# Optimization experiments

Hardware: AMD Instinct MI355X
Metric: run time of the kernel (lower is better)

Reference implementation:

```python
import jax, jax.numpy as jnp
import numpy as np

B, T, D_MODEL, H = 2, 2048, 1024, 16
D_HEAD = D_MODEL // H


def setup_inputs() -> dict:
    key = jax.random.key(0)
    k1, k2, k3 = jax.random.split(key, 3)
    x = jax.random.normal(k1, (B, T, D_MODEL), dtype=jnp.float32)
    # Linear weights stored as (in, out); scale like torch default init roughly
    W_qkv = jax.random.normal(k2, (D_MODEL, 3 * D_MODEL), dtype=jnp.float32) / np.sqrt(D_MODEL)
    W_o = jax.random.normal(k3, (D_MODEL, D_MODEL), dtype=jnp.float32) / np.sqrt(D_MODEL)
    return {"x": x, "W_qkv": W_qkv, "W_o": W_o}


def reference(x, W_qkv, W_o):
    Bx, Tx, C = x.shape
    qkv = x @ W_qkv                                   # (B,T,3C)
    qkv = qkv.reshape(Bx, Tx, 3, H, D_HEAD)
    q = qkv[:, :, 0].transpose(0, 2, 1, 3)            # (B,H,T,D)
    k = qkv[:, :, 1].transpose(0, 2, 1, 3)
    v = qkv[:, :, 2].transpose(0, 2, 1, 3)
    scale = 1.0 / np.sqrt(D_HEAD).astype(np.float32)
    att = jnp.einsum('bhqd,bhkd->bhqk', q, k) * scale  # (B,H,T,T)
    causal = jnp.tril(jnp.ones((Tx, Tx), dtype=bool))
    att = jnp.where(causal[None, None], att, jnp.float32(-jnp.inf))
    w = jax.nn.softmax(att, axis=-1)
    out = jnp.einsum('bhqk,bhkd->bhqd', w, v)          # (B,H,T,D)
    out = out.transpose(0, 2, 1, 3).reshape(Bx, Tx, C)
    return out @ W_o
```

## Files before the change

kernel.cpp:

```cpp
#include <hip/hip_runtime.h>

typedef unsigned short u16;
typedef unsigned int u32;
typedef __bf16 bf16x8 __attribute__((ext_vector_type(8)));
typedef float f32x4 __attribute__((ext_vector_type(4)));

#define DEV __device__ __forceinline__

constexpr int BB = 2;
constexpr int TT = 2048;
constexpr int CD = 1024;
constexpr int HH = 16;
constexpr int DH = 64;
constexpr int BT = BB * TT;

#define QSCALE 0.18033688011112042f

DEV u16 f2bf(float f) {
    u32 u = __builtin_bit_cast(u32, f);
    u32 r = u + 0x7FFFu + ((u >> 16) & 1u);
    return (u16)(r >> 16);
}

DEV f32x4 mfma16(bf16x8 a, bf16x8 b, f32x4 c) {
    return __builtin_amdgcn_mfma_f32_16x16x32_bf16(a, b, c, 0, 0, 0);
}

DEV void gld_lds16(u16* lds, const u16* g) {
    __builtin_amdgcn_global_load_lds(
        (const __attribute__((address_space(1))) unsigned int*)g,
        (__attribute__((address_space(3))) unsigned int*)lds, 16, 0, 0);
}

__global__ __launch_bounds__(256)
void prep_kernel(const float* __restrict__ x, u16* __restrict__ xb,
                 const float* __restrict__ Wqkv, u16* __restrict__ WqkvT,
                 const float* __restrict__ Wo, u16* __restrict__ WoT) {
    const int tid = threadIdx.x;
    int blk = blockIdx.x;
    if (blk < 2048) {
        const int i = (blk * 256 + tid) * 8;
        float4 a = *(const float4*)&x[i];
        float4 b = *(const float4*)&x[i + 4];
        u16 t[8];
        t[0] = f2bf(a.x); t[1] = f2bf(a.y); t[2] = f2bf(a.z); t[3] = f2bf(a.w);
        t[4] = f2bf(b.x); t[5] = f2bf(b.y); t[6] = f2bf(b.z); t[7] = f2bf(b.w);
        *(uint4*)&xb[i] = *(const uint4*)t;
        return;
    }
    __shared__ u16 tile[32][33];
    const float* in; u16* out; int rows, cols, bx, by;
    if (blk < 5120) { blk -= 2048; in = Wqkv; out = WqkvT; rows = 1024; cols = 3072; bx = blk % 96; by = blk / 96; }
    else            { blk -= 5120; in = Wo;   out = WoT;   rows = 1024; cols = 1024; bx = blk % 32; by = blk / 32; }
    const int c0 = bx * 32, r0 = by * 32;
    const int tx = tid & 31, ty = tid >> 5;
    #pragma unroll
    for (int i = ty; i < 32; i += 8)
        tile[i][tx] = f2bf(in[(r0 + i) * cols + (c0 + tx)]);
    __syncthreads();
    #pragma unroll
    for (int i = ty; i < 32; i += 8)
        out[(c0 + i) * rows + (r0 + tx)] = tile[tx][i];
}

template <int EPI, int BN, int GX>
__global__ __launch_bounds__(256)
void gemm_db(const u16* __restrict__ A, const u16* __restrict__ Bt,
             u16* __restrict__ out0, u16* __restrict__ out1,
             u16* __restrict__ out2, float* __restrict__ outf,
             int M, int N, int K) {
    constexpr int BM = 128, BK = 32, AST = 32;
    constexpr int NT = BN / 32;
    constexpr int NBLK = GX * 32;
    constexpr int CPX = NBLK / 8;
    __shared__ alignas(16) u16 As[2][BM * AST];
    __shared__ alignas(16) u16 Bs[2][BN * AST];

    const int tid  = threadIdx.x;
    const int wave = tid >> 6, lane = tid & 63;
    const int quad = lane >> 4, l16 = lane & 15;
    const int wm = (wave & 1) * 64, wn = (wave >> 1) * (BN / 2);

    int bid = (int)blockIdx.x;
    bid = (bid & 7) * CPX + (bid >> 3);
    const int bx = bid % GX, by = bid / GX;
    const int m0 = by * BM, n0 = bx * BN;

    const int srowA = wave * 32 + (lane >> 2);
    const int srowB = wave * (BN / 4) + (lane >> 2);
    const int scol  = (lane & 3) * 8;
    const u16* ga0 = A  + (size_t)(m0 + srowA) * K + scol;
    const u16* ga1 = ga0 + (size_t)16 * K;
    const u16* gb0 = Bt + (size_t)(n0 + srowB) * K + scol;
    const u16* gb1 = gb0 + (size_t)16 * K;

    auto stage = [&](int buf, int k0) {
        gld_lds16(&As[buf][wave * 1024],           ga0 + k0);
        gld_lds16(&As[buf][wave * 1024 + 512],     ga1 + k0);
        gld_lds16(&Bs[buf][wave * (BN * 8)],       gb0 + k0);
        if constexpr (BN == 128)
            gld_lds16(&Bs[buf][wave * (BN * 8) + 512], gb1 + k0);
    };

    f32x4 acc[4][NT] = {};

    stage(0, 0);
    __syncthreads();

    int cur = 0;
    for (int k0 = 0; k0 < K; k0 += BK, cur ^= 1) {
        if (k0 + BK < K) stage(cur ^ 1, k0 + BK);

        bf16x8 fa[4], fb[NT];
        #pragma unroll
        for (int mt = 0; mt < 4; ++mt)
            fa[mt] = *(const bf16x8*)&As[cur][(wm + mt * 16 + l16) * AST + quad * 8];
        #pragma unroll
        for (int nt = 0; nt < NT; ++nt)
            fb[nt] = *(const bf16x8*)&Bs[cur][(wn + nt * 16 + l16) * AST + quad * 8];
        #pragma unroll
        for (int mt = 0; mt < 4; ++mt)
            #pragma unroll
            for (int nt = 0; nt < NT; ++nt)
                acc[mt][nt] = mfma16(fa[mt], fb[nt], acc[mt][nt]);
        __syncthreads();
    }

    #pragma unroll
    for (int mt = 0; mt < 4; ++mt) {
        #pragma unroll
        for (int nt = 0; nt < NT; ++nt) {
            #pragma unroll
            for (int reg = 0; reg < 4; ++reg) {
                const int r = m0 + wm + mt * 16 + quad * 4 + reg;
                const int c = n0 + wn + nt * 16 + l16;
                if (EPI == 0) {
                    outf[(size_t)r * N + c] = acc[mt][nt][reg];
                } else {
                    const int which = c >> 10;
                    const int cc = c & 1023;
                    const int h = cc >> 6, d = cc & 63;
                    const int b = r >> 11, t = r & 2047;
                    const int bh = b * HH + h;
                    if (which == 0) {
                        out0[((size_t)bh * TT + t) * DH + d] =
                            f2bf(acc[mt][nt][reg] * QSCALE);
                    } else if (which == 1) {
                        out1[((size_t)bh * TT + t) * DH + d] = f2bf(acc[mt][nt][reg]);
                    } else {
                        out2[((size_t)bh * DH + d) * TT + t] = f2bf(acc[mt][nt][reg]);
                    }
                }
            }
        }
    }
}

constexpr int KST = 72;

DEV void attn_step(const bf16x8 fk[4][2], const bf16x8 fv[2][4],
                   const bf16x8* fq, f32x4* Oacc,
                   float& m_i, float& l_i, bool diag,
                   int wave, int quad, int l16) {
    f32x4 st[4];
    #pragma unroll
    for (int nt = 0; nt < 4; ++nt) {
        f32x4 t = {};
        t = mfma16(fk[nt][0], fq[0], t);
        t = mfma16(fk[nt][1], fq[1], t);
        st[nt] = t;
    }

    if (diag) {
        const int qg = wave * 16 + l16;
        #pragma unroll
        for (int nt = 0; nt < 4; ++nt)
            #pragma unroll
            for (int reg = 0; reg < 4; ++reg) {
                const int kg = nt * 16 + quad * 4 + reg;
                st[nt][reg] = (kg <= qg) ? st[nt][reg] : -INFINITY;
            }
    }

    float vmax = st[0][0];
    #pragma unroll
    for (int nt = 0; nt < 4; ++nt)
        #pragma unroll
        for (int reg = 0; reg < 4; ++reg)
            vmax = fmaxf(vmax, st[nt][reg]);
    vmax = fmaxf(vmax, __shfl_xor(vmax, 16, 64));
    vmax = fmaxf(vmax, __shfl_xor(vmax, 32, 64));

    const float mnew = fmaxf(m_i, vmax);
    const float alpha = __builtin_amdgcn_exp2f(m_i - mnew);
    m_i = mnew;

    float vsum = 0.f;
    #pragma unroll
    for (int nt = 0; nt < 4; ++nt)
        #pragma unroll
        for (int reg = 0; reg < 4; ++reg) {
            const float p = __builtin_amdgcn_exp2f(st[nt][reg] - mnew);
            st[nt][reg] = p;
            vsum += p;
        }
    vsum += __shfl_xor(vsum, 16, 64);
    vsum += __shfl_xor(vsum, 32, 64);
    l_i = l_i * alpha + vsum;

    #pragma unroll
    for (int dt = 0; dt < 4; ++dt)
        #pragma unroll
        for (int reg = 0; reg < 4; ++reg)
            Oacc[dt][reg] *= alpha;

    #pragma unroll
    for (int pair = 0; pair < 2; ++pair) {
        u16 pa[8];
        #pragma unroll
        for (int j = 0; j < 4; ++j) {
            pa[j]     = f2bf(st[2 * pair][j]);
            pa[4 + j] = f2bf(st[2 * pair + 1][j]);
        }
        const bf16x8 pb = *(const bf16x8*)pa;
        #pragma unroll
        for (int dt = 0; dt < 4; ++dt)
            Oacc[dt] = mfma16(fv[pair][dt], pb, Oacc[dt]);
    }
}

__global__ __launch_bounds__(256, 2)
void attn_kernel(const u16* __restrict__ Q, const u16* __restrict__ Kb,
                 const u16* __restrict__ Vt, u16* __restrict__ O) {
    __shared__ alignas(16) u16 Ks[2][64 * KST];
    __shared__ alignas(16) u16 Vs[2][64 * KST];

    const int p = blockIdx.x;
    const int bh = blockIdx.y;
    const int qtA = 31 - p;
    const int qtB = p;
    const int jmax = qtA;

    const int tid = threadIdx.x;
    const int wave = tid >> 6, lane = tid & 63;
    const int quad = lane >> 4, l16 = lane & 15;

    const u16* Qh = Q  + (size_t)bh * TT * DH;
    const u16* Kh = Kb + (size_t)bh * TT * DH;
    const u16* Vh = Vt + (size_t)bh * DH * TT;

    const int rowA = qtA * 64 + wave * 16;
    const int rowB = qtB * 64 + wave * 16;

    bf16x8 fqA[2], fqB[2];
    fqA[0] = *(const bf16x8*)&Qh[(rowA + l16) * DH + quad * 8];
    fqA[1] = *(const bf16x8*)&Qh[(rowA + l16) * DH + 32 + quad * 8];
    fqB[0] = *(const bf16x8*)&Qh[(rowB + l16) * DH + quad * 8];
    fqB[1] = *(const bf16x8*)&Qh[(rowB + l16) * DH + 32 + quad * 8];

    f32x4 OA[4] = {}, OB[4] = {};
    float mA = -INFINITY, lA = 0.f, mB = -INFINITY, lB = 0.f;

    const int trow = tid >> 3;
    const int ic   = tid & 7;
    const int tcol = ic * 8;
    const int vc1 = 32 * (ic >> 2) + 16 * (ic & 1) + 4 * ((ic & 3) >> 1);
    uint4 kr0, kr1, vr0, vr1;

    auto load_chunk = [&](int j) {
        const u16* ks = Kh + (size_t)j * 64 * DH;
        kr0 = *(const uint4*)&ks[trow * DH + tcol];
        kr1 = *(const uint4*)&ks[(trow + 32) * DH + tcol];
        const u16* vs = Vh + (size_t)j * 64;
        vr0 = *(const uint4*)&vs[(size_t)trow * TT + tcol];
        vr1 = *(const uint4*)&vs[(size_t)(trow + 32) * TT + tcol];
    };
    auto write_chunk = [&](int buf) {
        *(uint4*)&Ks[buf][trow * KST + tcol]        = kr0;
        *(uint4*)&Ks[buf][(trow + 32) * KST + tcol] = kr1;
        *(uint2*)&Vs[buf][trow * KST + vc1]            = *(const uint2*)&vr0;
        *(uint2*)&Vs[buf][trow * KST + vc1 + 8]        = *((const uint2*)&vr0 + 1);
        *(uint2*)&Vs[buf][(trow + 32) * KST + vc1]     = *(const uint2*)&vr1;
        *(uint2*)&Vs[buf][(trow + 32) * KST + vc1 + 8] = *((const uint2*)&vr1 + 1);
    };

    load_chunk(0);
    write_chunk(0);

    for (int j = 0; j <= jmax; ++j) {
        const int cur = j & 1;
        __syncthreads();
        if (j < jmax) load_chunk(j + 1);

        bf16x8 fk[4][2], fv[2][4];
        #pragma unroll
        for (int nt = 0; nt < 4; ++nt) {
            fk[nt][0] = *(const bf16x8*)&Ks[cur][(nt * 16 + l16) * KST + quad * 8];
            fk[nt][1] = *(const bf16x8*)&Ks[cur][(nt * 16 + l16) * KST + 32 + quad * 8];
        }
        #pragma unroll
        for (int pair = 0; pair < 2; ++pair)
            #pragma unroll
            for (int dt = 0; dt < 4; ++dt)
                fv[pair][dt] = *(const bf16x8*)
                    &Vs[cur][(dt * 16 + l16) * KST + pair * 32 + quad * 8];

        attn_step(fk, fv, fqA, OA, mA, lA, (j == qtA), wave, quad, l16);
        if (j <= qtB)
            attn_step(fk, fv, fqB, OB, mB, lB, (j == qtB), wave, quad, l16);
        if (j < jmax) write_chunk(cur ^ 1);
    }

    const int b = bh >> 4, h = bh & 15;
    const float rA = 1.f / lA, rB = 1.f / lB;
    #pragma unroll
    for (int dt = 0; dt < 4; ++dt) {
        u16 oa[4], ob[4];
        #pragma unroll
        for (int reg = 0; reg < 4; ++reg) {
            oa[reg] = f2bf(OA[dt][reg] * rA);
            ob[reg] = f2bf(OB[dt][reg] * rB);
        }
        *(uint2*)&O[((size_t)(b * TT + rowA + l16)) * CD + h * DH + dt * 16 + quad * 4] =
            *(const uint2*)oa;
        *(uint2*)&O[((size_t)(b * TT + rowB + l16)) * CD + h * DH + dt * 16 + quad * 4] =
            *(const uint2*)ob;
    }
}

extern "C" void kernel_launch(void* const* d_in, const int* in_sizes, int n_in,
                              void* d_out, int out_size, void* d_ws, size_t ws_size,
                              hipStream_t stream) {
    (void)in_sizes; (void)n_in; (void)out_size; (void)ws_size;
    const float* x    = (const float*)d_in[0];
    const float* Wqkv = (const float*)d_in[1];
    const float* Wo   = (const float*)d_in[2];
    float* out = (float*)d_out;

    char* ws = (char*)d_ws;
    u16* xb    = (u16*)(ws + 0);
    u16* WqkvT = (u16*)(ws + (8u  << 20));
    u16* WoT   = (u16*)(ws + (14u << 20));
    u16* Qb    = (u16*)(ws + (16u << 20));
    u16* Kb    = (u16*)(ws + (24u << 20));
    u16* Vt    = (u16*)(ws + (32u << 20));
    u16* attn  = (u16*)(ws + (40u << 20));

    prep_kernel<<<6144, 256, 0, stream>>>(x, xb, Wqkv, WqkvT, Wo, WoT);

    gemm_db<1, 128, 24><<<768, 256, 0, stream>>>(
        xb, WqkvT, Qb, Kb, Vt, nullptr, BT, 3072, CD);

    attn_kernel<<<dim3(16, BB * HH), 256, 0, stream>>>(Qb, Kb, Vt, attn);

    gemm_db<0, 64, 16><<<512, 256, 0, stream>>>(
        attn, WoT, nullptr, nullptr, nullptr, out, BT, CD, CD);
}
```

Before: 185.9 us.

## Split paired-tile attention blocks into single-tile blocks ordered longest-first

The attention kernel stops pairing two query tiles (qt and 31-qt) per block. It launches 1024 single-tile blocks, ordered so the longest causal tiles go first, and interleaves heads across block indices. Launch bounds go from 2 to 4 blocks per CU to raise occupancy. The softmax max and sum reductions become tree reductions to shorten dependency chains, and the float-to-bf16 conversion uses the native cast. This trades the K/V chunk reuse that came from sharing loads across two tiles for more parallelism and load balance through scheduling order, and it risks register pressure under the tighter launch bound.

```diff
diff --git a/kernel.cpp b/kernel.cpp
--- a/kernel.cpp
+++ b/kernel.cpp
@@ -17,9 +17,7 @@
 #define QSCALE 0.18033688011112042f
 
 DEV u16 f2bf(float f) {
-    u32 u = __builtin_bit_cast(u32, f);
-    u32 r = u + 0x7FFFu + ((u >> 16) & 1u);
-    return (u16)(r >> 16);
+    return __builtin_bit_cast(u16, (__bf16)f);
 }
 
 DEV f32x4 mfma16(bf16x8 a, bf16x8 b, f32x4 c) {
@@ -182,12 +180,18 @@
             }
     }
 
-    float vmax = st[0][0];
+    float v[16];
     #pragma unroll
     for (int nt = 0; nt < 4; ++nt)
         #pragma unroll
         for (int reg = 0; reg < 4; ++reg)
-            vmax = fmaxf(vmax, st[nt][reg]);
+            v[nt * 4 + reg] = st[nt][reg];
+    #pragma unroll
+    for (int s = 8; s > 0; s >>= 1)
+        #pragma unroll
+        for (int i = 0; i < s; ++i)
+            v[i] = fmaxf(v[i], v[i + s]);
+    float vmax = v[0];
     vmax = fmaxf(vmax, __shfl_xor(vmax, 16, 64));
     vmax = fmaxf(vmax, __shfl_xor(vmax, 32, 64));
 
@@ -195,15 +199,20 @@
     const float alpha = __builtin_amdgcn_exp2f(m_i - mnew);
     m_i = mnew;
 
-    float vsum = 0.f;
     #pragma unroll
     for (int nt = 0; nt < 4; ++nt)
         #pragma unroll
         for (int reg = 0; reg < 4; ++reg) {
             const float p = __builtin_amdgcn_exp2f(st[nt][reg] - mnew);
             st[nt][reg] = p;
-            vsum += p;
+            v[nt * 4 + reg] = p;
         }
+    #pragma unroll
+    for (int s = 8; s > 0; s >>= 1)
+        #pragma unroll
+        for (int i = 0; i < s; ++i)
+            v[i] += v[i + s];
+    float vsum = v[0];
     vsum += __shfl_xor(vsum, 16, 64);
     vsum += __shfl_xor(vsum, 32, 64);
     l_i = l_i * alpha + vsum;
@@ -216,30 +225,29 @@
 
     #pragma unroll
     for (int pair = 0; pair < 2; ++pair) {
-        u16 pa[8];
+        bf16x8 pb;
         #pragma unroll
         for (int j = 0; j < 4; ++j) {
-            pa[j]     = f2bf(st[2 * pair][j]);
-            pa[4 + j] = f2bf(st[2 * pair + 1][j]);
+            pb[j]     = (__bf16)st[2 * pair][j];
+            pb[4 + j] = (__bf16)st[2 * pair + 1][j];
         }
-        const bf16x8 pb = *(const bf16x8*)pa;
         #pragma unroll
         for (int dt = 0; dt < 4; ++dt)
             Oacc[dt] = mfma16(fv[pair][dt], pb, Oacc[dt]);
     }
 }
 
-__global__ __launch_bounds__(256, 2)
+__global__ __launch_bounds__(256, 4)
 void attn_kernel(const u16* __restrict__ Q, const u16* __restrict__ Kb,
                  const u16* __restrict__ Vt, u16* __restrict__ O) {
     __shared__ alignas(16) u16 Ks[2][64 * KST];
     __shared__ alignas(16) u16 Vs[2][64 * KST];
 
-    const int p = blockIdx.x;
-    const int bh = blockIdx.y;
-    const int qtA = 31 - p;
-    const int qtB = p;
-    const int jmax = qtA;
+    const int bid = (int)blockIdx.x;
+    const int j2 = bid >> 3;
+    const int qt = 31 - (j2 >> 2);
+    const int bh = (bid & 7) + 8 * (j2 & 3);
+    const int jmax = qt;
 
     const int tid = threadIdx.x;
     const int wave = tid >> 6, lane = tid & 63;
@@ -249,17 +257,14 @@
     const u16* Kh = Kb + (size_t)bh * TT * DH;
     const u16* Vh = Vt + (size_t)bh * DH * TT;
 
-    const int rowA = qtA * 64 + wave * 16;
-    const int rowB = qtB * 64 + wave * 16;
-
-    bf16x8 fqA[2], fqB[2];
-    fqA[0] = *(const bf16x8*)&Qh[(rowA + l16) * DH + quad * 8];
-    fqA[1] = *(const bf16x8*)&Qh[(rowA + l16) * DH + 32 + quad * 8];
-    fqB[0] = *(const bf16x8*)&Qh[(rowB + l16) * DH + quad * 8];
-    fqB[1] = *(const bf16x8*)&Qh[(rowB + l16) * DH + 32 + quad * 8];
-
-    f32x4 OA[4] = {}, OB[4] = {};
-    float mA = -INFINITY, lA = 0.f, mB = -INFINITY, lB = 0.f;
+    const int row = qt * 64 + wave * 16;
+
+    bf16x8 fq[2];
+    fq[0] = *(const bf16x8*)&Qh[(row + l16) * DH + quad * 8];
+    fq[1] = *(const bf16x8*)&Qh[(row + l16) * DH + 32 + quad * 8];
+
+    f32x4 Oa[4] = {};
+    float m_i = -INFINITY, l_i = 0.f;
 
     const int trow = tid >> 3;
     const int ic   = tid & 7;
@@ -305,26 +310,20 @@
                 fv[pair][dt] = *(const bf16x8*)
                     &Vs[cur][(dt * 16 + l16) * KST + pair * 32 + quad * 8];
 
-        attn_step(fk, fv, fqA, OA, mA, lA, (j == qtA), wave, quad, l16);
-        if (j <= qtB)
-            attn_step(fk, fv, fqB, OB, mB, lB, (j == qtB), wave, quad, l16);
+        attn_step(fk, fv, fq, Oa, m_i, l_i, (j == qt), wave, quad, l16);
         if (j < jmax) write_chunk(cur ^ 1);
     }
 
     const int b = bh >> 4, h = bh & 15;
-    const float rA = 1.f / lA, rB = 1.f / lB;
+    const float r_i = 1.f / l_i;
     #pragma unroll
     for (int dt = 0; dt < 4; ++dt) {
-        u16 oa[4], ob[4];
-        #pragma unroll
-        for (int reg = 0; reg < 4; ++reg) {
-            oa[reg] = f2bf(OA[dt][reg] * rA);
-            ob[reg] = f2bf(OB[dt][reg] * rB);
-        }
-        *(uint2*)&O[((size_t)(b * TT + rowA + l16)) * CD + h * DH + dt * 16 + quad * 4] =
+        u16 oa[4];
+        #pragma unroll
+        for (int reg = 0; reg < 4; ++reg)
+            oa[reg] = f2bf(Oa[dt][reg] * r_i);
+        *(uint2*)&O[((size_t)(b * TT + row + l16)) * CD + h * DH + dt * 16 + quad * 4] =
             *(const uint2*)oa;
-        *(uint2*)&O[((size_t)(b * TT + rowB + l16)) * CD + h * DH + dt * 16 + quad * 4] =
-            *(const uint2*)ob;
     }
 }
 
@@ -351,7 +350,7 @@
     gemm_db<1, 128, 24><<<768, 256, 0, stream>>>(
         xb, WqkvT, Qb, Kb, Vt, nullptr, BT, 3072, CD);
 
-    attn_kernel<<<dim3(16, BB * HH), 256, 0, stream>>>(Qb, Kb, Vt, attn);
+    attn_kernel<<<1024, 256, 0, stream>>>(Qb, Kb, Vt, attn);
 
     gemm_db<0, 64, 16><<<512, 256, 0, stream>>>(
         attn, WoT, nullptr, nullptr, nullptr, out, BT, CD, CD);
```

Result: faster. 177.6 us (-4.5%).
